# Kernel tuning notes

Hardware: AMD Instinct MI355X
Metric: run time of the kernel (lower is better)

## Reference

```python
import jax, jax.numpy as jnp
import numpy as np

D = 512
H = 4
DK = D // H
N_ACTOR = 4096
N_BV = 4096
NEG = jnp.float32(-1e9)  # stands in for -inf; exp underflows to exactly 0 in fp32


def setup_inputs() -> dict:
    key = jax.random.key(0)
    k1, k2, k3, k4, k5, k6, k7, k8 = jax.random.split(key, 8)
    a_z = jax.random.normal(k1, (N_ACTOR, D), dtype=jnp.float32)
    bv_z = jax.random.normal(k2, (N_BV, D), dtype=jnp.float32)
    mask = jax.random.uniform(k3, (N_ACTOR, N_BV)) > 0.5
    weight = jax.random.normal(k4, (N_ACTOR, N_BV), dtype=jnp.float32)
    # nn.MultiheadAttention parameters (packed in_proj, out_proj)
    in_proj_w = jax.random.normal(k5, (3 * D, D), dtype=jnp.float32) * 0.02
    in_proj_b = jax.random.normal(k6, (3 * D,), dtype=jnp.float32) * 0.02
    out_w = jax.random.normal(k7, (D, D), dtype=jnp.float32) * 0.02
    out_b = jax.random.normal(k8, (D,), dtype=jnp.float32) * 0.02
    return {"a_z": a_z, "bv_z": bv_z, "mask": mask, "weight": weight,
            "in_proj_w": in_proj_w, "in_proj_b": in_proj_b,
            "out_w": out_w, "out_b": out_b}


def reference(a_z, bv_z, mask, weight, in_proj_w, in_proj_b, out_w, out_b):
    n, d = a_z.shape
    m = bv_z.shape[0]
    a = jnp.nan_to_num(a_z, nan=0.0, posinf=1.0, neginf=-1.0)
    kv = jnp.nan_to_num(bv_z, nan=0.0, posinf=1.0, neginf=-1.0)
    w = jnp.nan_to_num(weight, nan=0.0, posinf=1.0, neginf=-1.0)
    mf = mask.astype(a.dtype)
    valid = jnp.any(mask, axis=1)  # actors with at least one unmasked key

    # attn_mask = weight masked with -inf at padded keys (covers key_padding_mask too)
    bias = jnp.where(mask, w, NEG)  # [n, m]

    wq, wk, wv = jnp.split(in_proj_w, 3, axis=0)
    bq, bk, bv = jnp.split(in_proj_b, 3, axis=0)
    q = ((a @ wq.T + bq).reshape(n, H, DK)) * (1.0 / np.sqrt(DK))
    k = (kv @ wk.T + bk).reshape(m, H, DK)
    v = (kv @ wv.T + bv).reshape(m, H, DK)

    scores = jnp.einsum('nhd,mhd->nhm', q, k) + bias[:, None, :]
    attn = jax.nn.softmax(scores, axis=-1)                  # [n, h, m]
    ctx = jnp.einsum('nhm,mhd->nhd', attn, v).reshape(n, d)
    out = ctx @ out_w.T + out_b                              # out_proj

    # topic alignment: mean over head-chunks of the projected output
    topic = out.reshape(n, H, DK).mean(axis=1)               # [n, dk]

    # influence: softmax-normalized weight scores dotted with avg attn weights
    aw = attn.mean(axis=1) * mf                              # head-averaged attn, masked
    norm_scores = jax.nn.softmax(bias, axis=-1) * mf
    influence = jnp.sum(norm_scores * aw, axis=-1)           # [n]

    # actors with no valid key are scattered back as zeros
    topic = jnp.where(valid[:, None], topic, 0.0)
    influence = jnp.where(valid, influence, 0.0)
    return topic, influence
```

## Files before the change

kernel.cpp:

```cpp
#include <hip/hip_runtime.h>
#include <hip/hip_bf16.h>
#include <cstdint>
#include <cstddef>


typedef __attribute__((ext_vector_type(8))) short bf16x8;
typedef __attribute__((ext_vector_type(4))) short bf16x4;
typedef __attribute__((ext_vector_type(4))) float f32x4;

#define MFMA32(a, b, c) __builtin_amdgcn_mfma_f32_16x16x32_bf16((a), (b), (c), 0, 0, 0)
#define MFMA16(a, b, c) __builtin_amdgcn_mfma_f32_16x16x16bf16_1k((a), (b), (c), 0, 0, 0)

static __device__ __forceinline__ short f2b(float x) {
  union { float f; unsigned u; } v; v.f = x;
  unsigned r = v.u + 0x7fffu + ((v.u >> 16) & 1u);
  return (short)(r >> 16);
}

__global__ __launch_bounds__(256) void k_qkv(
    const float* __restrict__ a, const float* __restrict__ kv,
    const float* __restrict__ w, const float* __restrict__ bias,
    short* __restrict__ Qb, short* __restrict__ Kp, short* __restrict__ Vp)
{
  __shared__ short As[128 * 40];
  __shared__ short Bs[64 * 40];
  const int blk = blockIdx.x;
  const int bm = blk % 32, bn = blk / 32;
  const int m0 = bm * 128, n0 = bn * 64;
  const float* __restrict__ Ain = (bn < 8) ? a : kv;
  const int tid = threadIdx.x;
  const int lane = tid & 63, wvi = tid >> 6;
  const int wm = (wvi >> 1) * 64, wn = (wvi & 1) * 32;
  const int c = lane & 15, g = lane >> 4;
  const int srA = tid >> 1, scA = (tid & 1) * 16;
  const int srB = tid >> 2, scB = (tid & 3) * 8;

  f32x4 acc[4][2];
#pragma unroll
  for (int i = 0; i < 4; ++i)
#pragma unroll
    for (int j = 0; j < 2; ++j) acc[i][j] = (f32x4)0.f;

  for (int k0 = 0; k0 < 512; k0 += 32) {
    const float* ap = Ain + (size_t)(m0 + srA) * 512 + k0 + scA;
#pragma unroll
    for (int j = 0; j < 4; ++j) {
      f32x4 av = *(const f32x4*)(ap + 4 * j);
      bf16x4 as;
      as.x = f2b(av.x); as.y = f2b(av.y); as.z = f2b(av.z); as.w = f2b(av.w);
      *(bf16x4*)(&As[srA * 40 + scA + 4 * j]) = as;
    }
    const float* bp = w + (size_t)(n0 + srB) * 512 + k0 + scB;
#pragma unroll
    for (int j = 0; j < 2; ++j) {
      f32x4 bv = *(const f32x4*)(bp + 4 * j);
      bf16x4 bs;
      bs.x = f2b(bv.x); bs.y = f2b(bv.y); bs.z = f2b(bv.z); bs.w = f2b(bv.w);
      *(bf16x4*)(&Bs[srB * 40 + scB + 4 * j]) = bs;
    }
    __syncthreads();
    bf16x8 af[4], bfg[2];
#pragma unroll
    for (int t = 0; t < 4; ++t)
      af[t] = *(const bf16x8*)(&As[(wm + t * 16 + c) * 40 + g * 8]);
#pragma unroll
    for (int t = 0; t < 2; ++t)
      bfg[t] = *(const bf16x8*)(&Bs[(wn + t * 16 + c) * 40 + g * 8]);
#pragma unroll
    for (int rt = 0; rt < 4; ++rt)
#pragma unroll
      for (int ct = 0; ct < 2; ++ct)
        acc[rt][ct] = MFMA32(af[rt], bfg[ct], acc[rt][ct]);
    __syncthreads();
  }

#pragma unroll
  for (int ct = 0; ct < 2; ++ct) {
    const int col = n0 + wn + ct * 16 + c;
    const float bj = bias[col];
#pragma unroll
    for (int rt = 0; rt < 4; ++rt) {
      const int row = m0 + wm + rt * 16 + g * 4;
      const int mc = row >> 4;
      if (col < 512) {
#pragma unroll
        for (int r = 0; r < 4; ++r)
          Qb[(size_t)(row + r) * 512 + col] = f2b((acc[rt][ct][r] + bj) * 0.08838834764831843f);
      } else if (col < 1024) {
        const int colK = col - 512;
        const int h = colK >> 7, dk = colK & 127;
        const int ks = dk >> 5, gk = (dk >> 3) & 3, j = dk & 7;
        short* base = Kp + (size_t)((((h * 256 + mc) * 4 + ks) * 64) + gk * 16 + g * 4) * 8 + j;
#pragma unroll
        for (int r = 0; r < 4; ++r) base[r * 8] = f2b(acc[rt][ct][r] + bj);
      } else {
        const int colV = col - 1024;
        const int h = colV >> 7, db = (colV & 127) >> 4, cv = colV & 15;
        bf16x4 pk;
#pragma unroll
        for (int r = 0; r < 4; ++r) pk[r] = f2b(acc[rt][ct][r] + bj);
        *(bf16x4*)(Vp + (size_t)((((h * 256 + mc) * 8 + db) * 64) + g * 16 + cv) * 4) = pk;
      }
    }
  }
}

__global__ __launch_bounds__(256) void k_pre(
    const int* __restrict__ msk, const float* __restrict__ wgt,
    float* __restrict__ Ep)
{
  const int b = blockIdx.x;
  const int rb = b >> 3, ks8 = b & 7;
  const int t = threadIdx.x;
  const int c = t >> 4;
  const int row = rb * 16 + c;
  const int lt = t & 15;
  const int g = t & 3;
#pragma unroll
  for (int p = 0; p < 8; ++p) {
    const int k0 = ks8 * 512 + p * 64 + lt * 4;
    const int4 mk = *(const int4*)(msk + (size_t)row * 4096 + k0);
    const f32x4 wv = *(const f32x4*)(wgt + (size_t)row * 4096 + k0);
    f32x4 ev;
    ev[0] = mk.x ? __expf(wv.x) : 0.f;
    ev[1] = mk.y ? __expf(wv.y) : 0.f;
    ev[2] = mk.z ? __expf(wv.z) : 0.f;
    ev[3] = mk.w ? __expf(wv.w) : 0.f;
    const int mc = k0 >> 4;
    *(f32x4*)(Ep + ((size_t)(rb * 256 + mc) * 64 + g * 16 + c) * 4) = ev;
  }
}

template<int EP>
__global__ __launch_bounds__(256, 4) void k_attn(
    const short* __restrict__ Qb, const short* __restrict__ Kp,
    const short* __restrict__ Vp, const float* __restrict__ wgt,
    const int* __restrict__ msk, const int S,
    short* __restrict__ Opart, float* __restrict__ lpart,
    float* __restrict__ cipart, float* __restrict__ lbpart,
    const float* __restrict__ Ep)
{
  const int bx = blockIdx.x;
  const int sp = bx % S, rb = bx / S;
  const int n0 = rb * 16;
  const int mlen = 4096 / S;
  const int mc0 = (sp * mlen) >> 4;
  const int nch = mlen >> 4;
  const int tid = threadIdx.x;
  const int lane = tid & 63, h = tid >> 6;
  const int c = lane & 15, g = lane >> 4;

  bf16x8 qf[4];
#pragma unroll
  for (int ks = 0; ks < 4; ++ks)
    qf[ks] = *(const bf16x8*)(Qb + (size_t)(n0 + c) * 512 + h * 128 + ks * 32 + g * 8);

  f32x4 O[8];
#pragma unroll
  for (int db = 0; db < 8; ++db) O[db] = (f32x4)0.f;
  float lh = 0.f, lb = 0.f, ci = 0.f;

  const short* Kw = Kp + (size_t)h * 524288 + (size_t)lane * 8 + (size_t)mc0 * 2048;
  const short* Vw = Vp + (size_t)h * 524288 + (size_t)lane * 4 + (size_t)mc0 * 2048;

  if (EP) {
    const float* Eb = Ep + ((size_t)(rb * 256 + mc0) * 64 + lane) * 4;
    f32x4 evC = *(const f32x4*)(Eb);
    for (int t = 0; t < nch; ++t) {
      bf16x8 kf[4];
#pragma unroll
      for (int ks = 0; ks < 4; ++ks)
        kf[ks] = *(const bf16x8*)(Kw + t * 2048 + ks * 512);
      bf16x4 vf[8];
#pragma unroll
      for (int db = 0; db < 8; ++db)
        vf[db] = *(const bf16x4*)(Vw + t * 2048 + db * 256);
      const f32x4 ev = evC;
      const int tn = (t + 1 < nch) ? (t + 1) : t;
      evC = *(const f32x4*)(Eb + (size_t)tn * 256);

      f32x4 Sa = (f32x4)0.f, Sb = (f32x4)0.f;
      Sa = MFMA32(kf[0], qf[0], Sa);
      Sb = MFMA32(kf[2], qf[2], Sb);
      Sa = MFMA32(kf[1], qf[1], Sa);
      Sb = MFMA32(kf[3], qf[3], Sb);
      const float p0 = __expf(Sa[0] + Sb[0]) * ev[0];
      const float p1 = __expf(Sa[1] + Sb[1]) * ev[1];
      const float p2 = __expf(Sa[2] + Sb[2]) * ev[2];
      const float p3 = __expf(Sa[3] + Sb[3]) * ev[3];
      lh += (p0 + p1) + (p2 + p3);
      lb += (ev[0] + ev[1]) + (ev[2] + ev[3]);
      ci += (p0 * ev[0] + p1 * ev[1]) + (p2 * ev[2] + p3 * ev[3]);
      bf16x4 pa;
      pa[0] = f2b(p0); pa[1] = f2b(p1); pa[2] = f2b(p2); pa[3] = f2b(p3);
#pragma unroll
      for (int db = 0; db < 8; ++db)
        O[db] = MFMA16(pa, vf[db], O[db]);
    }
  } else {
    const int* mbase_p = msk + (size_t)(n0 + c) * 4096 + g * 4 + (size_t)mc0 * 16;
    const float* wbase_p = wgt + (size_t)(n0 + c) * 4096 + g * 4 + (size_t)mc0 * 16;
    int4 mkN = *(const int4*)(mbase_p);
    f32x4 wvN = *(const f32x4*)(wbase_p);
    for (int t = 0; t < nch; ++t) {
      bf16x8 kf[4];
#pragma unroll
      for (int ks = 0; ks < 4; ++ks)
        kf[ks] = *(const bf16x8*)(Kw + t * 2048 + ks * 512);
      bf16x4 vf[8];
#pragma unroll
      for (int db = 0; db < 8; ++db)
        vf[db] = *(const bf16x4*)(Vw + t * 2048 + db * 256);
      const int4 mkC = mkN;
      const f32x4 wvC = wvN;
      const int tn = (t + 1 < nch) ? (t + 1) : t;
      mkN = *(const int4*)(mbase_p + tn * 16);
      wvN = *(const f32x4*)(wbase_p + tn * 16);
      f32x4 Sv = (f32x4)0.f;
#pragma unroll
      for (int ks = 0; ks < 4; ++ks) Sv = MFMA32(kf[ks], qf[ks], Sv);
      const float e0 = mkC.x ? __expf(wvC.x) : 0.f;
      const float e1 = mkC.y ? __expf(wvC.y) : 0.f;
      const float e2 = mkC.z ? __expf(wvC.z) : 0.f;
      const float e3 = mkC.w ? __expf(wvC.w) : 0.f;
      const float p0 = __expf(Sv[0]) * e0, p1 = __expf(Sv[1]) * e1;
      const float p2 = __expf(Sv[2]) * e2, p3 = __expf(Sv[3]) * e3;
      lh += (p0 + p1) + (p2 + p3);
      lb += (e0 + e1) + (e2 + e3);
      ci += (p0 * e0 + p1 * e1) + (p2 * e2 + p3 * e3);
      bf16x4 pa;
      pa[0] = f2b(p0); pa[1] = f2b(p1); pa[2] = f2b(p2); pa[3] = f2b(p3);
#pragma unroll
      for (int db = 0; db < 8; ++db)
        O[db] = MFMA16(pa, vf[db], O[db]);
    }
  }

  lh += __shfl_xor(lh, 16, 64); lh += __shfl_xor(lh, 32, 64);
  lb += __shfl_xor(lb, 16, 64); lb += __shfl_xor(lb, 32, 64);
  ci += __shfl_xor(ci, 16, 64); ci += __shfl_xor(ci, 32, 64);

  float inv[4];
#pragma unroll
  for (int r = 0; r < 4; ++r)
    inv[r] = 1.f / fmaxf(__shfl(lh, 4 * g + r, 64), 1e-30f);
#pragma unroll
  for (int db = 0; db < 8; ++db)
#pragma unroll
    for (int r = 0; r < 4; ++r)
      Opart[(size_t)sp * (4096 * 512) + (size_t)(n0 + g * 4 + r) * 512 +
            h * 128 + db * 16 + c] = f2b(O[db][r] * inv[r]);

  if (g == 0) {
    const int row = n0 + c;
    lpart[((size_t)sp * 4 + h) * 4096 + row] = lh;
    cipart[((size_t)sp * 4 + h) * 4096 + row] = ci;
    if (h == 0) lbpart[(size_t)sp * 4096 + row] = lb;
  }
}

__global__ __launch_bounds__(256) void k_comb(
    const short* __restrict__ Opart, const float* __restrict__ lpart,
    const float* __restrict__ cipart, const float* __restrict__ lbpart,
    const int S, short* __restrict__ ctxb, float* __restrict__ validw,
    float* __restrict__ infl)
{
  const int tid = threadIdx.x;
  const int rloc = tid >> 5, cseg = tid & 31;
  const int row = blockIdx.x * 8 + rloc;
  const int col0 = cseg * 16;
  const int h = col0 >> 7;

  float l[4], ciS[4], lb = 0.f;
#pragma unroll
  for (int hh = 0; hh < 4; ++hh) { l[hh] = 0.f; ciS[hh] = 0.f; }
  for (int s = 0; s < S; ++s) {
#pragma unroll
    for (int hh = 0; hh < 4; ++hh) {
      l[hh]   += lpart[((size_t)s * 4 + hh) * 4096 + row];
      ciS[hh] += cipart[((size_t)s * 4 + hh) * 4096 + row];
    }
    lb += lbpart[(size_t)s * 4096 + row];
  }

  float acc[16];
#pragma unroll
  for (int j = 0; j < 16; ++j) acc[j] = 0.f;
  const float linv = 1.f / fmaxf(l[h], 1e-30f);
  for (int s = 0; s < S; ++s) {
    const float w_s = lpart[((size_t)s * 4 + h) * 4096 + row] * linv;
    const bf16x8 o0 = *(const bf16x8*)(Opart + (size_t)s * (4096 * 512) + (size_t)row * 512 + col0);
    const bf16x8 o1 = *(const bf16x8*)(Opart + (size_t)s * (4096 * 512) + (size_t)row * 512 + col0 + 8);
#pragma unroll
    for (int j = 0; j < 8; ++j) {
      union { unsigned u; float f; } v0, v1;
      v0.u = ((unsigned)(unsigned short)o0[j]) << 16;
      v1.u = ((unsigned)(unsigned short)o1[j]) << 16;
      acc[j]     += w_s * v0.f;
      acc[8 + j] += w_s * v1.f;
    }
  }
  bf16x8 c0, c1;
#pragma unroll
  for (int j = 0; j < 8; ++j) { c0[j] = f2b(acc[j]); c1[j] = f2b(acc[8 + j]); }
  *(bf16x8*)(ctxb + (size_t)row * 512 + col0) = c0;
  *(bf16x8*)(ctxb + (size_t)row * 512 + col0 + 8) = c1;

  if (cseg == 0) {
    validw[row] = (lb > 0.f) ? 1.f : 0.f;
    float s_ = 0.f;
#pragma unroll
    for (int hh = 0; hh < 4; ++hh) s_ += ciS[hh] / fmaxf(l[hh], 1e-30f);
    infl[row] = (lb > 0.f) ? s_ / (4.f * lb) : 0.f;
  }
}

__global__ void k_fold(const float* __restrict__ ow, const float* __restrict__ ob,
                       short* __restrict__ Wf, float* __restrict__ bfo)
{
  const int idx = blockIdx.x * 256 + threadIdx.x;
  if (idx < 128 * 512) {
    const int dk = idx >> 9, d = idx & 511;
    const float s = 0.25f * (ow[(size_t)dk * 512 + d] + ow[(size_t)(dk + 128) * 512 + d] +
                             ow[(size_t)(dk + 256) * 512 + d] + ow[(size_t)(dk + 384) * 512 + d]);
    Wf[(size_t)dk * 512 + d] = f2b(s);
  }
  if (idx < 128) bfo[idx] = 0.25f * (ob[idx] + ob[idx + 128] + ob[idx + 256] + ob[idx + 384]);
}

__global__ __launch_bounds__(256) void k_out(
    const short* __restrict__ ctxb, const short* __restrict__ Wf,
    const float* __restrict__ bfo, const float* __restrict__ validw,
    float* __restrict__ topic)
{
  const int tid = threadIdx.x;
  const int lane = tid & 63, wvi = tid >> 6;
  const int m0 = blockIdx.x * 16;
  const int c = lane & 15, g = lane >> 4;

  f32x4 acc[2];
  acc[0] = (f32x4)0.f; acc[1] = (f32x4)0.f;

  for (int k0 = 0; k0 < 512; k0 += 32) {
    const bf16x8 af = *(const bf16x8*)(ctxb + (size_t)(m0 + c) * 512 + k0 + g * 8);
#pragma unroll
    for (int dbl = 0; dbl < 2; ++dbl) {
      const bf16x8 bfr = *(const bf16x8*)(Wf + (size_t)(wvi * 32 + dbl * 16 + c) * 512 + k0 + g * 8);
      acc[dbl] = MFMA32(af, bfr, acc[dbl]);
    }
  }

#pragma unroll
  for (int r = 0; r < 4; ++r) {
    const int row = m0 + g * 4 + r;
    const float va = validw[row];
#pragma unroll
    for (int dbl = 0; dbl < 2; ++dbl) {
      const int col = wvi * 32 + dbl * 16 + c;
      const float vl = (va > 0.5f) ? (acc[dbl][r] + bfo[col]) : 0.f;
      topic[(size_t)row * 128 + col] = vl;
    }
  }
}

extern "C" void kernel_launch(void* const* d_in, const int* in_sizes, int n_in,
                              void* d_out, int out_size, void* d_ws, size_t ws_size,
                              hipStream_t stream) {
  const float* a_z  = (const float*)d_in[0];
  const float* bv_z = (const float*)d_in[1];
  const int*   mask = (const int*)d_in[2];
  const float* wgt  = (const float*)d_in[3];
  const float* ipw  = (const float*)d_in[4];
  const float* ipb  = (const float*)d_in[5];
  const float* ow   = (const float*)d_in[6];
  const float* ob   = (const float*)d_in[7];
  float* topic = (float*)d_out;
  float* infl  = (float*)d_out + 4096 * 128;

  const size_t MB = (size_t)1 << 20;
  char* ws = (char*)d_ws;
  short* Qb     = (short*)(ws);
  short* Kp     = (short*)(ws + 4 * MB);
  short* Vp     = (short*)(ws + 8 * MB);
  short* ctxb   = (short*)(ws + 12 * MB);
  float* validw = (float*)(ws + 16 * MB);
  short* Wf     = (short*)(ws + 16 * MB + (64 << 10));
  float* bfo    = (float*)(ws + 16 * MB + (224 << 10));
  const size_t fixed = 16 * MB + (256 << 10);
  const size_t epBytes = (size_t)4096 * 4096 * 4;

  auto need = [&](int S, int ep) {
    return fixed + (ep ? epBytes : 0) + (size_t)S * (4 * MB + (144 << 10));
  };
  int S = 8, useEp = 1;
  while (S > 1 && need(S, 1) > ws_size) S >>= 1;
  if (need(S, 1) > ws_size) {
    useEp = 0; S = 8;
    while (S > 1 && need(S, 0) > ws_size) S >>= 1;
  }
  float* Ep = useEp ? (float*)(ws + fixed) : nullptr;
  char* pbase = ws + fixed + (useEp ? epBytes : 0);
  short* Opart  = (short*)(pbase);
  float* lpart  = (float*)(pbase + (size_t)S * 4 * MB);
  float* cipart = (float*)(pbase + (size_t)S * 4 * MB + ((size_t)S << 16));
  float* lbpart = (float*)(pbase + (size_t)S * 4 * MB + ((size_t)S << 17));

  k_qkv <<<768, 256, 0, stream>>>(a_z, bv_z, ipw, ipb, Qb, Kp, Vp);
  k_fold<<<256, 256, 0, stream>>>(ow, ob, Wf, bfo);
  if (useEp) {
    k_pre<<<2048, 256, 0, stream>>>(mask, wgt, Ep);
    k_attn<1><<<256 * S, 256, 0, stream>>>(Qb, Kp, Vp, wgt, mask, S,
                                           Opart, lpart, cipart, lbpart, Ep);
  } else {
    k_attn<0><<<256 * S, 256, 0, stream>>>(Qb, Kp, Vp, wgt, mask, S,
                                           Opart, lpart, cipart, lbpart, Ep);
  }
  k_comb<<<512, 256, 0, stream>>>(Opart, lpart, cipart, lbpart, S, ctxb, validw, infl);
  k_out <<<256, 256, 0, stream>>>(ctxb, Wf, bfo, validw, topic);
}
```

Baseline: 330.4 us.

## Merge QKV, mask-exp and fold kernels; double-buffer K loads in attention loop

```diff
diff --git a/kernel.cpp b/kernel.cpp
--- a/kernel.cpp
+++ b/kernel.cpp
@@ -17,119 +17,160 @@
   return (short)(r >> 16);
 }
 
-__global__ __launch_bounds__(256) void k_qkv(
+__global__ __launch_bounds__(256) void k_front(
     const float* __restrict__ a, const float* __restrict__ kv,
     const float* __restrict__ w, const float* __restrict__ bias,
-    short* __restrict__ Qb, short* __restrict__ Kp, short* __restrict__ Vp)
+    short* __restrict__ Qb, short* __restrict__ Kp, short* __restrict__ Vp,
+    const int* __restrict__ msk, const float* __restrict__ wgt,
+    float* __restrict__ Ep,
+    const float* __restrict__ ow, const float* __restrict__ ob,
+    short* __restrict__ Wf, float* __restrict__ bfo, const int useEp)
 {
   __shared__ short As[128 * 40];
   __shared__ short Bs[64 * 40];
   const int blk = blockIdx.x;
-  const int bm = blk % 32, bn = blk / 32;
-  const int m0 = bm * 128, n0 = bn * 64;
-  const float* __restrict__ Ain = (bn < 8) ? a : kv;
   const int tid = threadIdx.x;
-  const int lane = tid & 63, wvi = tid >> 6;
-  const int wm = (wvi >> 1) * 64, wn = (wvi & 1) * 32;
-  const int c = lane & 15, g = lane >> 4;
-  const int srA = tid >> 1, scA = (tid & 1) * 16;
-  const int srB = tid >> 2, scB = (tid & 3) * 8;
-
-  f32x4 acc[4][2];
-#pragma unroll
-  for (int i = 0; i < 4; ++i)
-#pragma unroll
-    for (int j = 0; j < 2; ++j) acc[i][j] = (f32x4)0.f;
-
-  for (int k0 = 0; k0 < 512; k0 += 32) {
-    const float* ap = Ain + (size_t)(m0 + srA) * 512 + k0 + scA;
-#pragma unroll
-    for (int j = 0; j < 4; ++j) {
-      f32x4 av = *(const f32x4*)(ap + 4 * j);
-      bf16x4 as;
-      as.x = f2b(av.x); as.y = f2b(av.y); as.z = f2b(av.z); as.w = f2b(av.w);
-      *(bf16x4*)(&As[srA * 40 + scA + 4 * j]) = as;
-    }
-    const float* bp = w + (size_t)(n0 + srB) * 512 + k0 + scB;
-#pragma unroll
-    for (int j = 0; j < 2; ++j) {
-      f32x4 bv = *(const f32x4*)(bp + 4 * j);
-      bf16x4 bs;
-      bs.x = f2b(bv.x); bs.y = f2b(bv.y); bs.z = f2b(bv.z); bs.w = f2b(bv.w);
-      *(bf16x4*)(&Bs[srB * 40 + scB + 4 * j]) = bs;
-    }
-    __syncthreads();
-    bf16x8 af[4], bfg[2];
-#pragma unroll
-    for (int t = 0; t < 4; ++t)
-      af[t] = *(const bf16x8*)(&As[(wm + t * 16 + c) * 40 + g * 8]);
-#pragma unroll
-    for (int t = 0; t < 2; ++t)
-      bfg[t] = *(const bf16x8*)(&Bs[(wn + t * 16 + c) * 40 + g * 8]);
-#pragma unroll
-    for (int rt = 0; rt < 4; ++rt)
-#pragma unroll
-      for (int ct = 0; ct < 2; ++ct)
-        acc[rt][ct] = MFMA32(af[rt], bfg[ct], acc[rt][ct]);
-    __syncthreads();
-  }
-
-#pragma unroll
-  for (int ct = 0; ct < 2; ++ct) {
-    const int col = n0 + wn + ct * 16 + c;
-    const float bj = bias[col];
-#pragma unroll
-    for (int rt = 0; rt < 4; ++rt) {
-      const int row = m0 + wm + rt * 16 + g * 4;
-      const int mc = row >> 4;
-      if (col < 512) {
-#pragma unroll
-        for (int r = 0; r < 4; ++r)
-          Qb[(size_t)(row + r) * 512 + col] = f2b((acc[rt][ct][r] + bj) * 0.08838834764831843f);
-      } else if (col < 1024) {
-        const int colK = col - 512;
-        const int h = colK >> 7, dk = colK & 127;
-        const int ks = dk >> 5, gk = (dk >> 3) & 3, j = dk & 7;
-        short* base = Kp + (size_t)((((h * 256 + mc) * 4 + ks) * 64) + gk * 16 + g * 4) * 8 + j;
-#pragma unroll
-        for (int r = 0; r < 4; ++r) base[r * 8] = f2b(acc[rt][ct][r] + bj);
-      } else {
-        const int colV = col - 1024;
-        const int h = colV >> 7, db = (colV & 127) >> 4, cv = colV & 15;
-        bf16x4 pk;
-#pragma unroll
-        for (int r = 0; r < 4; ++r) pk[r] = f2b(acc[rt][ct][r] + bj);
-        *(bf16x4*)(Vp + (size_t)((((h * 256 + mc) * 8 + db) * 64) + g * 16 + cv) * 4) = pk;
+
+  if (blk < 768) {
+    const int bm = blk % 32, bn = blk / 32;
+    const int m0 = bm * 128, n0 = bn * 64;
+    const float* __restrict__ Ain = (bn < 8) ? a : kv;
+    const int lane = tid & 63, wvi = tid >> 6;
+    const int wm = (wvi >> 1) * 64, wn = (wvi & 1) * 32;
+    const int c = lane & 15, g = lane >> 4;
+    const int srA = tid >> 1, scA = (tid & 1) * 16;
+    const int srB = tid >> 2, scB = (tid & 3) * 8;
+
+    f32x4 acc[4][2];
+#pragma unroll
+    for (int i = 0; i < 4; ++i)
+#pragma unroll
+      for (int j = 0; j < 2; ++j) acc[i][j] = (f32x4)0.f;
+
+    for (int k0 = 0; k0 < 512; k0 += 32) {
+      const float* ap = Ain + (size_t)(m0 + srA) * 512 + k0 + scA;
+#pragma unroll
+      for (int j = 0; j < 4; ++j) {
+        f32x4 av = *(const f32x4*)(ap + 4 * j);
+        bf16x4 as;
+        as.x = f2b(av.x); as.y = f2b(av.y); as.z = f2b(av.z); as.w = f2b(av.w);
+        *(bf16x4*)(&As[srA * 40 + scA + 4 * j]) = as;
       }
-    }
-  }
-}
-
-__global__ __launch_bounds__(256) void k_pre(
-    const int* __restrict__ msk, const float* __restrict__ wgt,
-    float* __restrict__ Ep)
-{
-  const int b = blockIdx.x;
-  const int rb = b >> 3, ks8 = b & 7;
-  const int t = threadIdx.x;
-  const int c = t >> 4;
-  const int row = rb * 16 + c;
-  const int lt = t & 15;
-  const int g = t & 3;
-#pragma unroll
-  for (int p = 0; p < 8; ++p) {
-    const int k0 = ks8 * 512 + p * 64 + lt * 4;
-    const int4 mk = *(const int4*)(msk + (size_t)row * 4096 + k0);
-    const f32x4 wv = *(const f32x4*)(wgt + (size_t)row * 4096 + k0);
-    f32x4 ev;
-    ev[0] = mk.x ? __expf(wv.x) : 0.f;
-    ev[1] = mk.y ? __expf(wv.y) : 0.f;
-    ev[2] = mk.z ? __expf(wv.z) : 0.f;
-    ev[3] = mk.w ? __expf(wv.w) : 0.f;
-    const int mc = k0 >> 4;
-    *(f32x4*)(Ep + ((size_t)(rb * 256 + mc) * 64 + g * 16 + c) * 4) = ev;
-  }
-}
+      const float* bp = w + (size_t)(n0 + srB) * 512 + k0 + scB;
+#pragma unroll
+      for (int j = 0; j < 2; ++j) {
+        f32x4 bv = *(const f32x4*)(bp + 4 * j);
+        bf16x4 bs;
+        bs.x = f2b(bv.x); bs.y = f2b(bv.y); bs.z = f2b(bv.z); bs.w = f2b(bv.w);
+        *(bf16x4*)(&Bs[srB * 40 + scB + 4 * j]) = bs;
+      }
+      __syncthreads();
+      bf16x8 af[4], bfg[2];
+#pragma unroll
+      for (int t = 0; t < 4; ++t)
+        af[t] = *(const bf16x8*)(&As[(wm + t * 16 + c) * 40 + g * 8]);
+#pragma unroll
+      for (int t = 0; t < 2; ++t)
+        bfg[t] = *(const bf16x8*)(&Bs[(wn + t * 16 + c) * 40 + g * 8]);
+#pragma unroll
+      for (int rt = 0; rt < 4; ++rt)
+#pragma unroll
+        for (int ct = 0; ct < 2; ++ct)
+          acc[rt][ct] = MFMA32(af[rt], bfg[ct], acc[rt][ct]);
+      __syncthreads();
+    }
+
+#pragma unroll
+    for (int ct = 0; ct < 2; ++ct) {
+      const int col = n0 + wn + ct * 16 + c;
+      const float bj = bias[col];
+#pragma unroll
+      for (int rt = 0; rt < 4; ++rt) {
+        const int row = m0 + wm + rt * 16 + g * 4;
+        const int mc = row >> 4;
+        if (col < 512) {
+#pragma unroll
+          for (int r = 0; r < 4; ++r)
+            Qb[(size_t)(row + r) * 512 + col] = f2b((acc[rt][ct][r] + bj) * 0.08838834764831843f);
+        } else if (col < 1024) {
+          const int colK = col - 512;
+          const int h = colK >> 7, dk = colK & 127;
+          const int ks = dk >> 5, gk = (dk >> 3) & 3, j = dk & 7;
+          short* base = Kp + (size_t)((((h * 256 + mc) * 4 + ks) * 64) + gk * 16 + g * 4) * 8 + j;
+#pragma unroll
+          for (int r = 0; r < 4; ++r) base[r * 8] = f2b(acc[rt][ct][r] + bj);
+        } else {
+          const int colV = col - 1024;
+          const int h = colV >> 7, db = (colV & 127) >> 4, cv = colV & 15;
+          bf16x4 pk;
+#pragma unroll
+          for (int r = 0; r < 4; ++r) pk[r] = f2b(acc[rt][ct][r] + bj);
+          *(bf16x4*)(Vp + (size_t)((((h * 256 + mc) * 8 + db) * 64) + g * 16 + cv) * 4) = pk;
+        }
+      }
+    }
+  } else if (blk < 2816) {
+    if (!useEp) return;
+    const int b = blk - 768;
+    const int rb = b >> 3, ks8 = b & 7;
+    const int c = tid >> 4;
+    const int row = rb * 16 + c;
+    const int lt = tid & 15;
+    const int g = tid & 3;
+#pragma unroll
+    for (int p = 0; p < 8; ++p) {
+      const int k0 = ks8 * 512 + p * 64 + lt * 4;
+      const int4 mk = *(const int4*)(msk + (size_t)row * 4096 + k0);
+      const f32x4 wv = *(const f32x4*)(wgt + (size_t)row * 4096 + k0);
+      f32x4 ev;
+      ev[0] = mk.x ? __expf(wv.x) : 0.f;
+      ev[1] = mk.y ? __expf(wv.y) : 0.f;
+      ev[2] = mk.z ? __expf(wv.z) : 0.f;
+      ev[3] = mk.w ? __expf(wv.w) : 0.f;
+      const int mc = k0 >> 4;
+      *(f32x4*)(Ep + ((size_t)(rb * 256 + mc) * 64 + g * 16 + c) * 4) = ev;
+    }
+  } else {
+    const int idx = (blk - 2816) * 256 + tid;
+    if (idx < 128 * 512) {
+      const int dk = idx >> 9, d = idx & 511;
+      const float s = 0.25f * (ow[(size_t)dk * 512 + d] + ow[(size_t)(dk + 128) * 512 + d] +
+                               ow[(size_t)(dk + 256) * 512 + d] + ow[(size_t)(dk + 384) * 512 + d]);
+      Wf[(size_t)dk * 512 + d] = f2b(s);
+    }
+    if (idx < 128) bfo[idx] = 0.25f * (ob[idx] + ob[idx + 128] + ob[idx + 256] + ob[idx + 384]);
+  }
+}
+
+#define ASTEP(TT, KC, KN, TN)                                                  \
+  do {                                                                         \
+    bf16x4 vf[8];                                                              \
+    _Pragma("unroll")                                                          \
+    for (int db = 0; db < 8; ++db)                                             \
+      vf[db] = *(const bf16x4*)(Vw + (TT) * 2048 + db * 256);                  \
+    const f32x4 ev = evC;                                                      \
+    evC = *(const f32x4*)(Eb + (size_t)(TN) * 256);                            \
+    _Pragma("unroll")                                                          \
+    for (int ks = 0; ks < 4; ++ks)                                             \
+      KN[ks] = *(const bf16x8*)(Kw + (TN) * 2048 + ks * 512);                  \
+    f32x4 Sa = (f32x4)0.f, Sb = (f32x4)0.f;                                    \
+    Sa = MFMA32(KC[0], qf[0], Sa);                                             \
+    Sb = MFMA32(KC[2], qf[2], Sb);                                             \
+    Sa = MFMA32(KC[1], qf[1], Sa);                                             \
+    Sb = MFMA32(KC[3], qf[3], Sb);                                             \
+    const float p0 = __expf(Sa[0] + Sb[0]) * ev[0];                            \
+    const float p1 = __expf(Sa[1] + Sb[1]) * ev[1];                            \
+    const float p2 = __expf(Sa[2] + Sb[2]) * ev[2];                            \
+    const float p3 = __expf(Sa[3] + Sb[3]) * ev[3];                            \
+    lh += (p0 + p1) + (p2 + p3);                                               \
+    lb += (ev[0] + ev[1]) + (ev[2] + ev[3]);                                   \
+    ci += (p0 * ev[0] + p1 * ev[1]) + (p2 * ev[2] + p3 * ev[3]);               \
+    bf16x4 pa;                                                                 \
+    pa[0] = f2b(p0); pa[1] = f2b(p1); pa[2] = f2b(p2); pa[3] = f2b(p3);        \
+    _Pragma("unroll")                                                          \
+    for (int db = 0; db < 8; ++db)                                             \
+      O[db] = MFMA16(pa, vf[db], O[db]);                                       \
+  } while (0)
 
 template<int EP>
 __global__ __launch_bounds__(256, 4) void k_attn(
@@ -166,36 +207,14 @@
   if (EP) {
     const float* Eb = Ep + ((size_t)(rb * 256 + mc0) * 64 + lane) * 4;
     f32x4 evC = *(const f32x4*)(Eb);
-    for (int t = 0; t < nch; ++t) {
-      bf16x8 kf[4];
-#pragma unroll
-      for (int ks = 0; ks < 4; ++ks)
-        kf[ks] = *(const bf16x8*)(Kw + t * 2048 + ks * 512);
-      bf16x4 vf[8];
-#pragma unroll
-      for (int db = 0; db < 8; ++db)
-        vf[db] = *(const bf16x4*)(Vw + t * 2048 + db * 256);
-      const f32x4 ev = evC;
-      const int tn = (t + 1 < nch) ? (t + 1) : t;
-      evC = *(const f32x4*)(Eb + (size_t)tn * 256);
-
-      f32x4 Sa = (f32x4)0.f, Sb = (f32x4)0.f;
-      Sa = MFMA32(kf[0], qf[0], Sa);
-      Sb = MFMA32(kf[2], qf[2], Sb);
-      Sa = MFMA32(kf[1], qf[1], Sa);
-      Sb = MFMA32(kf[3], qf[3], Sb);
-      const float p0 = __expf(Sa[0] + Sb[0]) * ev[0];
-      const float p1 = __expf(Sa[1] + Sb[1]) * ev[1];
-      const float p2 = __expf(Sa[2] + Sb[2]) * ev[2];
-      const float p3 = __expf(Sa[3] + Sb[3]) * ev[3];
-      lh += (p0 + p1) + (p2 + p3);
-      lb += (ev[0] + ev[1]) + (ev[2] + ev[3]);
-      ci += (p0 * ev[0] + p1 * ev[1]) + (p2 * ev[2] + p3 * ev[3]);
-      bf16x4 pa;
-      pa[0] = f2b(p0); pa[1] = f2b(p1); pa[2] = f2b(p2); pa[3] = f2b(p3);
-#pragma unroll
-      for (int db = 0; db < 8; ++db)
-        O[db] = MFMA16(pa, vf[db], O[db]);
+    bf16x8 kA[4], kB[4];
+#pragma unroll
+    for (int ks = 0; ks < 4; ++ks)
+      kA[ks] = *(const bf16x8*)(Kw + ks * 512);
+    for (int t = 0; t < nch; t += 2) {
+      ASTEP(t, kA, kB, t + 1);
+      const int tn2 = (t + 2 < nch) ? (t + 2) : (nch - 1);
+      ASTEP(t + 1, kB, kA, tn2);
     }
   } else {
     const int* mbase_p = msk + (size_t)(n0 + c) * 4096 + g * 4 + (size_t)mc0 * 16;
@@ -313,19 +332,6 @@
     for (int hh = 0; hh < 4; ++hh) s_ += ciS[hh] / fmaxf(l[hh], 1e-30f);
     infl[row] = (lb > 0.f) ? s_ / (4.f * lb) : 0.f;
   }
-}
-
-__global__ void k_fold(const float* __restrict__ ow, const float* __restrict__ ob,
-                       short* __restrict__ Wf, float* __restrict__ bfo)
-{
-  const int idx = blockIdx.x * 256 + threadIdx.x;
-  if (idx < 128 * 512) {
-    const int dk = idx >> 9, d = idx & 511;
-    const float s = 0.25f * (ow[(size_t)dk * 512 + d] + ow[(size_t)(dk + 128) * 512 + d] +
-                             ow[(size_t)(dk + 256) * 512 + d] + ow[(size_t)(dk + 384) * 512 + d]);
-    Wf[(size_t)dk * 512 + d] = f2b(s);
-  }
-  if (idx < 128) bfo[idx] = 0.25f * (ob[idx] + ob[idx + 128] + ob[idx + 256] + ob[idx + 384]);
 }
 
 __global__ __launch_bounds__(256) void k_out(
@@ -405,10 +411,9 @@
   float* cipart = (float*)(pbase + (size_t)S * 4 * MB + ((size_t)S << 16));
   float* lbpart = (float*)(pbase + (size_t)S * 4 * MB + ((size_t)S << 17));
 
-  k_qkv <<<768, 256, 0, stream>>>(a_z, bv_z, ipw, ipb, Qb, Kp, Vp);
-  k_fold<<<256, 256, 0, stream>>>(ow, ob, Wf, bfo);
+  k_front<<<3072, 256, 0, stream>>>(a_z, bv_z, ipw, ipb, Qb, Kp, Vp,
+                                    mask, wgt, Ep, ow, ob, Wf, bfo, useEp);
   if (useEp) {
-    k_pre<<<2048, 256, 0, stream>>>(mask, wgt, Ep);
     k_attn<1><<<256 * S, 256, 0, stream>>>(Qb, Kp, Vp, wgt, mask, S,
                                            Opart, lpart, cipart, lbpart, Ep);
   } else {
```

Result: faster. 322.4 us (-2.4%).

## Merge QKV GEMM, mask-exp precompute and out-proj fold into one launch

Applied to the files above, without the earlier changes.

```diff
diff --git a/kernel.cpp b/kernel.cpp
--- a/kernel.cpp
+++ b/kernel.cpp
@@ -17,117 +17,124 @@
   return (short)(r >> 16);
 }
 
-__global__ __launch_bounds__(256) void k_qkv(
+__global__ __launch_bounds__(256) void k_front(
     const float* __restrict__ a, const float* __restrict__ kv,
     const float* __restrict__ w, const float* __restrict__ bias,
-    short* __restrict__ Qb, short* __restrict__ Kp, short* __restrict__ Vp)
+    short* __restrict__ Qb, short* __restrict__ Kp, short* __restrict__ Vp,
+    const int* __restrict__ msk, const float* __restrict__ wgt,
+    float* __restrict__ Ep,
+    const float* __restrict__ ow, const float* __restrict__ ob,
+    short* __restrict__ Wf, float* __restrict__ bfo, const int useEp)
 {
   __shared__ short As[128 * 40];
-  __shared__ short Bs[64 * 40];
+  __shared__ short Bs[128 * 40];
   const int blk = blockIdx.x;
-  const int bm = blk % 32, bn = blk / 32;
-  const int m0 = bm * 128, n0 = bn * 64;
-  const float* __restrict__ Ain = (bn < 8) ? a : kv;
   const int tid = threadIdx.x;
-  const int lane = tid & 63, wvi = tid >> 6;
-  const int wm = (wvi >> 1) * 64, wn = (wvi & 1) * 32;
-  const int c = lane & 15, g = lane >> 4;
-  const int srA = tid >> 1, scA = (tid & 1) * 16;
-  const int srB = tid >> 2, scB = (tid & 3) * 8;
-
-  f32x4 acc[4][2];
-#pragma unroll
-  for (int i = 0; i < 4; ++i)
-#pragma unroll
-    for (int j = 0; j < 2; ++j) acc[i][j] = (f32x4)0.f;
-
-  for (int k0 = 0; k0 < 512; k0 += 32) {
-    const float* ap = Ain + (size_t)(m0 + srA) * 512 + k0 + scA;
-#pragma unroll
-    for (int j = 0; j < 4; ++j) {
-      f32x4 av = *(const f32x4*)(ap + 4 * j);
-      bf16x4 as;
-      as.x = f2b(av.x); as.y = f2b(av.y); as.z = f2b(av.z); as.w = f2b(av.w);
-      *(bf16x4*)(&As[srA * 40 + scA + 4 * j]) = as;
-    }
-    const float* bp = w + (size_t)(n0 + srB) * 512 + k0 + scB;
-#pragma unroll
-    for (int j = 0; j < 2; ++j) {
-      f32x4 bv = *(const f32x4*)(bp + 4 * j);
-      bf16x4 bs;
-      bs.x = f2b(bv.x); bs.y = f2b(bv.y); bs.z = f2b(bv.z); bs.w = f2b(bv.w);
-      *(bf16x4*)(&Bs[srB * 40 + scB + 4 * j]) = bs;
-    }
-    __syncthreads();
-    bf16x8 af[4], bfg[2];
-#pragma unroll
-    for (int t = 0; t < 4; ++t)
-      af[t] = *(const bf16x8*)(&As[(wm + t * 16 + c) * 40 + g * 8]);
-#pragma unroll
-    for (int t = 0; t < 2; ++t)
-      bfg[t] = *(const bf16x8*)(&Bs[(wn + t * 16 + c) * 40 + g * 8]);
-#pragma unroll
-    for (int rt = 0; rt < 4; ++rt)
-#pragma unroll
-      for (int ct = 0; ct < 2; ++ct)
-        acc[rt][ct] = MFMA32(af[rt], bfg[ct], acc[rt][ct]);
-    __syncthreads();
-  }
-
-#pragma unroll
-  for (int ct = 0; ct < 2; ++ct) {
-    const int col = n0 + wn + ct * 16 + c;
-    const float bj = bias[col];
-#pragma unroll
-    for (int rt = 0; rt < 4; ++rt) {
-      const int row = m0 + wm + rt * 16 + g * 4;
-      const int mc = row >> 4;
-      if (col < 512) {
-#pragma unroll
-        for (int r = 0; r < 4; ++r)
-          Qb[(size_t)(row + r) * 512 + col] = f2b((acc[rt][ct][r] + bj) * 0.08838834764831843f);
-      } else if (col < 1024) {
-        const int colK = col - 512;
-        const int h = colK >> 7, dk = colK & 127;
-        const int ks = dk >> 5, gk = (dk >> 3) & 3, j = dk & 7;
-        short* base = Kp + (size_t)((((h * 256 + mc) * 4 + ks) * 64) + gk * 16 + g * 4) * 8 + j;
-#pragma unroll
-        for (int r = 0; r < 4; ++r) base[r * 8] = f2b(acc[rt][ct][r] + bj);
-      } else {
-        const int colV = col - 1024;
-        const int h = colV >> 7, db = (colV & 127) >> 4, cv = colV & 15;
-        bf16x4 pk;
-#pragma unroll
-        for (int r = 0; r < 4; ++r) pk[r] = f2b(acc[rt][ct][r] + bj);
-        *(bf16x4*)(Vp + (size_t)((((h * 256 + mc) * 8 + db) * 64) + g * 16 + cv) * 4) = pk;
+
+  if (blk < 384) {
+    const int bm = blk % 32, bn = blk / 32;
+    const int m0 = bm * 128, n0 = bn * 128;
+    const float* __restrict__ Ain = (bn < 4) ? a : kv;
+    const int lane = tid & 63, wvi = tid >> 6;
+    const int wm = (wvi >> 1) * 64, wn = (wvi & 1) * 64;
+    const int c = lane & 15, g = lane >> 4;
+    const int sr = tid >> 1, sc = (tid & 1) * 16;
+
+    f32x4 acc[4][4];
+#pragma unroll
+    for (int i = 0; i < 4; ++i)
+#pragma unroll
+      for (int j = 0; j < 4; ++j) acc[i][j] = (f32x4)0.f;
+
+    for (int k0 = 0; k0 < 512; k0 += 32) {
+      const float* ap = Ain + (size_t)(m0 + sr) * 512 + k0 + sc;
+      const float* bp = w + (size_t)(n0 + sr) * 512 + k0 + sc;
+#pragma unroll
+      for (int j = 0; j < 4; ++j) {
+        f32x4 av = *(const f32x4*)(ap + 4 * j);
+        bf16x4 as;
+        as.x = f2b(av.x); as.y = f2b(av.y); as.z = f2b(av.z); as.w = f2b(av.w);
+        *(bf16x4*)(&As[sr * 40 + sc + 4 * j]) = as;
+        f32x4 bv = *(const f32x4*)(bp + 4 * j);
+        bf16x4 bs;
+        bs.x = f2b(bv.x); bs.y = f2b(bv.y); bs.z = f2b(bv.z); bs.w = f2b(bv.w);
+        *(bf16x4*)(&Bs[sr * 40 + sc + 4 * j]) = bs;
       }
-    }
-  }
-}
-
-__global__ __launch_bounds__(256) void k_pre(
-    const int* __restrict__ msk, const float* __restrict__ wgt,
-    float* __restrict__ Ep)
-{
-  const int b = blockIdx.x;
-  const int rb = b >> 3, ks8 = b & 7;
-  const int t = threadIdx.x;
-  const int c = t >> 4;
-  const int row = rb * 16 + c;
-  const int lt = t & 15;
-  const int g = t & 3;
-#pragma unroll
-  for (int p = 0; p < 8; ++p) {
-    const int k0 = ks8 * 512 + p * 64 + lt * 4;
-    const int4 mk = *(const int4*)(msk + (size_t)row * 4096 + k0);
-    const f32x4 wv = *(const f32x4*)(wgt + (size_t)row * 4096 + k0);
-    f32x4 ev;
-    ev[0] = mk.x ? __expf(wv.x) : 0.f;
-    ev[1] = mk.y ? __expf(wv.y) : 0.f;
-    ev[2] = mk.z ? __expf(wv.z) : 0.f;
-    ev[3] = mk.w ? __expf(wv.w) : 0.f;
-    const int mc = k0 >> 4;
-    *(f32x4*)(Ep + ((size_t)(rb * 256 + mc) * 64 + g * 16 + c) * 4) = ev;
+      __syncthreads();
+      bf16x8 af[4], bfg[4];
+#pragma unroll
+      for (int t = 0; t < 4; ++t)
+        af[t] = *(const bf16x8*)(&As[(wm + t * 16 + c) * 40 + g * 8]);
+#pragma unroll
+      for (int t = 0; t < 4; ++t)
+        bfg[t] = *(const bf16x8*)(&Bs[(wn + t * 16 + c) * 40 + g * 8]);
+#pragma unroll
+      for (int rt = 0; rt < 4; ++rt)
+#pragma unroll
+        for (int ct = 0; ct < 4; ++ct)
+          acc[rt][ct] = MFMA32(af[rt], bfg[ct], acc[rt][ct]);
+      __syncthreads();
+    }
+
+#pragma unroll
+    for (int ct = 0; ct < 4; ++ct) {
+      const int col = n0 + wn + ct * 16 + c;
+      const float bj = bias[col];
+#pragma unroll
+      for (int rt = 0; rt < 4; ++rt) {
+        const int row = m0 + wm + rt * 16 + g * 4;
+        const int mc = row >> 4;
+        if (col < 512) {
+#pragma unroll
+          for (int r = 0; r < 4; ++r)
+            Qb[(size_t)(row + r) * 512 + col] = f2b((acc[rt][ct][r] + bj) * 0.08838834764831843f);
+        } else if (col < 1024) {
+          const int colK = col - 512;
+          const int h = colK >> 7, dk = colK & 127;
+          const int ks = dk >> 5, gk = (dk >> 3) & 3, j = dk & 7;
+          short* base = Kp + (size_t)((((h * 256 + mc) * 4 + ks) * 64) + gk * 16 + g * 4) * 8 + j;
+#pragma unroll
+          for (int r = 0; r < 4; ++r) base[r * 8] = f2b(acc[rt][ct][r] + bj);
+        } else {
+          const int colV = col - 1024;
+          const int h = colV >> 7, db = (colV & 127) >> 4, cv = colV & 15;
+          bf16x4 pk;
+#pragma unroll
+          for (int r = 0; r < 4; ++r) pk[r] = f2b(acc[rt][ct][r] + bj);
+          *(bf16x4*)(Vp + (size_t)((((h * 256 + mc) * 8 + db) * 64) + g * 16 + cv) * 4) = pk;
+        }
+      }
+    }
+  } else if (blk < 2432) {
+    if (!useEp) return;
+    const int b = blk - 384;
+    const int rb = b >> 3, ks8 = b & 7;
+    const int c = tid >> 4;
+    const int row = rb * 16 + c;
+    const int lt = tid & 15;
+    const int g = tid & 3;
+#pragma unroll
+    for (int p = 0; p < 8; ++p) {
+      const int k0 = ks8 * 512 + p * 64 + lt * 4;
+      const int4 mk = *(const int4*)(msk + (size_t)row * 4096 + k0);
+      const f32x4 wv = *(const f32x4*)(wgt + (size_t)row * 4096 + k0);
+      f32x4 ev;
+      ev[0] = mk.x ? __expf(wv.x) : 0.f;
+      ev[1] = mk.y ? __expf(wv.y) : 0.f;
+      ev[2] = mk.z ? __expf(wv.z) : 0.f;
+      ev[3] = mk.w ? __expf(wv.w) : 0.f;
+      const int mc = k0 >> 4;
+      *(f32x4*)(Ep + ((size_t)(rb * 256 + mc) * 64 + g * 16 + c) * 4) = ev;
+    }
+  } else {
+    const int idx = (blk - 2432) * 256 + tid;
+    if (idx < 128 * 512) {
+      const int dk = idx >> 9, d = idx & 511;
+      const float s = 0.25f * (ow[(size_t)dk * 512 + d] + ow[(size_t)(dk + 128) * 512 + d] +
+                               ow[(size_t)(dk + 256) * 512 + d] + ow[(size_t)(dk + 384) * 512 + d]);
+      Wf[(size_t)dk * 512 + d] = f2b(s);
+    }
+    if (idx < 128) bfo[idx] = 0.25f * (ob[idx] + ob[idx + 128] + ob[idx + 256] + ob[idx + 384]);
   }
 }
 
@@ -315,19 +322,6 @@
   }
 }
 
-__global__ void k_fold(const float* __restrict__ ow, const float* __restrict__ ob,
-                       short* __restrict__ Wf, float* __restrict__ bfo)
-{
-  const int idx = blockIdx.x * 256 + threadIdx.x;
-  if (idx < 128 * 512) {
-    const int dk = idx >> 9, d = idx & 511;
-    const float s = 0.25f * (ow[(size_t)dk * 512 + d] + ow[(size_t)(dk + 128) * 512 + d] +
-                             ow[(size_t)(dk + 256) * 512 + d] + ow[(size_t)(dk + 384) * 512 + d]);
-    Wf[(size_t)dk * 512 + d] = f2b(s);
-  }
-  if (idx < 128) bfo[idx] = 0.25f * (ob[idx] + ob[idx + 128] + ob[idx + 256] + ob[idx + 384]);
-}
-
 __global__ __launch_bounds__(256) void k_out(
     const short* __restrict__ ctxb, const short* __restrict__ Wf,
     const float* __restrict__ bfo, const float* __restrict__ validw,
@@ -405,10 +399,9 @@
   float* cipart = (float*)(pbase + (size_t)S * 4 * MB + ((size_t)S << 16));
   float* lbpart = (float*)(pbase + (size_t)S * 4 * MB + ((size_t)S << 17));
 
-  k_qkv <<<768, 256, 0, stream>>>(a_z, bv_z, ipw, ipb, Qb, Kp, Vp);
-  k_fold<<<256, 256, 0, stream>>>(ow, ob, Wf, bfo);
+  k_front<<<2688, 256, 0, stream>>>(a_z, bv_z, ipw, ipb, Qb, Kp, Vp,
+                                    mask, wgt, Ep, ow, ob, Wf, bfo, useEp);
   if (useEp) {
-    k_pre<<<2048, 256, 0, stream>>>(mask, wgt, Ep);
     k_attn<1><<<256 * S, 256, 0, stream>>>(Qb, Kp, Vp, wgt, mask, S,
                                            Opart, lpart, cipart, lbpart, Ep);
   } else {
```

Result: faster. 316.7 us (-4.1%).
